# Optimization experiments

Measured on AMD Instinct MI355X. Metric: run time of the kernel, lower is better.

Reference implementation:

```python
import jax, jax.numpy as jnp
import numpy as np

B, N, IN_DIM, OUT_DIM, E = 2, 100000, 128, 128, 600000


def setup_inputs() -> dict:
    key = jax.random.key(0)
    ks = jax.random.split(key, 16)
    inp = {
        'x': jax.random.normal(ks[0], (B, N, IN_DIM), dtype=jnp.float32),
        'edges_r0': jax.random.randint(ks[1], (2, E), 0, N, dtype=jnp.int64),
        'edges_r1': jax.random.randint(ks[2], (2, E), 0, N, dtype=jnp.int64),
        'edges_r2': jax.random.randint(ks[3], (2, E), 0, N, dtype=jnp.int64),
    }
    s = 1.0 / np.sqrt(IN_DIM)
    for i in range(3):
        inp[f'w{i}'] = jax.random.uniform(ks[4 + 3 * i], (OUT_DIM, IN_DIM), minval=-s, maxval=s, dtype=jnp.float32)
        inp[f'gw{i}'] = jax.random.uniform(ks[5 + 3 * i], (2 * OUT_DIM, IN_DIM), minval=-s, maxval=s, dtype=jnp.float32)
        inp[f'gb{i}'] = jax.random.uniform(ks[6 + 3 * i], (2 * OUT_DIM,), minval=-s, maxval=s, dtype=jnp.float32)
    return inp


def _film_conv(x, edges_list, w_list, gw_list, gb_list):
    # x: (B,N,F). For each relation: gather src/dst, linear, FiLM, scatter_add on dst.
    Bn, Nn, _ = x.shape
    out = jnp.zeros((Bn, Nn, OUT_DIM), dtype=x.dtype)
    for edge_index, w, gw, gb in zip(edges_list, w_list, gw_list, gb_list):
        src, dst = edge_index[0], edge_index[1]
        x_src = x[:, src, :]                       # (B,E,F)
        msg_lin = jnp.einsum('bef,of->beo', x_src, w)
        x_dst = x[:, dst, :]                       # (B,E,F)
        film = jnp.einsum('bef,of->beo', x_dst, gw) + gb
        omega, mu = film[..., :OUT_DIM], film[..., OUT_DIM:]
        msg = jax.nn.relu(jax.nn.sigmoid(omega) * msg_lin + mu)
        out = out.at[:, dst, :].add(msg)
    return out


def reference(x, edges_r0, edges_r1, edges_r2, w0, w1, w2, gw0, gb0, gw1, gb1, gw2, gb2):
    return _film_conv(x, [edges_r0, edges_r1, edges_r2], [w0, w1, w2],
                      [gw0, gw1, gw2], [gb0, gb1, gb2])
```

## Files before the change

### kernel.cpp

```cpp
#include <hip/hip_runtime.h>

#define Bn 2
#define Nn 100000
#define DIM 128
#define En 600000
#define MTOT (Bn * Nn)
#define DPB 32

typedef __attribute__((ext_vector_type(8))) short bf16x8;
typedef __attribute__((ext_vector_type(4))) float f32x4;

__device__ __forceinline__ unsigned short f2bf(float f) {
    union { float f; unsigned u; } v; v.f = f;
    unsigned r = v.u + 0x7fffu + ((v.u >> 16) & 1u);
    return (unsigned short)(r >> 16);
}
__device__ __forceinline__ float bf2f(unsigned u16) {
    union { unsigned u; float f; } v; v.u = u16 << 16; return v.f;
}
__device__ __forceinline__ float bf_lo(unsigned u) {
    union { unsigned u; float f; } v; v.u = u << 16; return v.f;
}
__device__ __forceinline__ float bf_hi(unsigned u) {
    union { unsigned u; float f; } v; v.u = u & 0xffff0000u; return v.f;
}

__global__ __launch_bounds__(256) void cvt_x_kernel(const float4* __restrict__ x,
                                                    ushort4* __restrict__ xbf) {
    int i = blockIdx.x * 256 + threadIdx.x;
    float4 v = x[i];
    ushort4 o;
    o.x = f2bf(v.x); o.y = f2bf(v.y); o.z = f2bf(v.z); o.w = f2bf(v.w);
    xbf[i] = o;
}

__global__ __launch_bounds__(256) void cvt_w_kernel(
    const float* __restrict__ w0,  const float* __restrict__ gw0,
    const float* __restrict__ w1,  const float* __restrict__ gw1,
    const float* __restrict__ w2,  const float* __restrict__ gw2,
    unsigned short* __restrict__ WB)
{
    int idx = blockIdx.x * 256 + threadIdx.x;
    int r = idx / 49152;
    int j = idx - r * 49152;
    const float* w  = (r == 0) ? w0  : (r == 1 ? w1  : w2);
    const float* gw = (r == 0) ? gw0 : (r == 1 ? gw1 : gw2);
    float v = (j < 128 * 128) ? w[j] : gw[j - 128 * 128];
    WB[idx] = f2bf(v);
}

__global__ __launch_bounds__(256) void count_kernel(
    const int* __restrict__ e0, const int* __restrict__ e1, const int* __restrict__ e2,
    int* __restrict__ counts)
{
    int idx = blockIdx.x * 256 + threadIdx.x;
    if (idx >= 3 * En) return;
    int r = (idx >= 2 * En) ? 2 : (idx >= En ? 1 : 0);
    int e = idx - r * En;
    const int* ed = (r == 0) ? e0 : (r == 1 ? e1 : e2);
    int dst = ed[En + e];
    atomicAdd(&counts[r * Nn + dst], 1);
}

#define WPR 1563
__global__ __launch_bounds__(256) void alloc_kernel(
    const int* __restrict__ counts,
    int* __restrict__ starts,
    int* __restrict__ gcursor)
{
    int wid  = blockIdx.x * 4 + (threadIdx.x >> 6);
    int lane = threadIdx.x & 63;
    int r = wid / WPR;
    if (r >= 3) return;
    int dst = (wid - r * WPR) * 64 + lane;
    int c = (dst < Nn) ? counts[r * Nn + dst] : 0;

    int inc = c;
#pragma unroll
    for (int d = 1; d < 64; d <<= 1) {
        int v = __shfl_up(inc, d);
        if (lane >= d) inc += v;
    }
    int total = __shfl(inc, 63);
    int base = 0;
    if (lane == 63) base = atomicAdd(&gcursor[r], total);
    base = __shfl(base, 63);

    if (dst < Nn) starts[r * Nn + dst] = base + inc - c;
}

__global__ __launch_bounds__(256) void fill_kernel(
    const int* __restrict__ e0, const int* __restrict__ e1, const int* __restrict__ e2,
    const int* __restrict__ starts,
    int* __restrict__ cursor,
    int* __restrict__ records)
{
    int idx = blockIdx.x * 256 + threadIdx.x;
    if (idx >= 3 * En) return;
    int r = (idx >= 2 * En) ? 2 : (idx >= En ? 1 : 0);
    int e = idx - r * En;
    const int* ed = (r == 0) ? e0 : (r == 1 ? e1 : e2);
    int src = ed[e];
    int dst = ed[En + e];
    int pos = atomicAdd(&cursor[r * Nn + dst], 1);
    records[(size_t)r * En + starts[r * Nn + dst] + pos] = src;
}

__global__ __launch_bounds__(256) void transformA_kernel(
    const short* __restrict__ Xbf,
    const short* __restrict__ WB,
    unsigned short* __restrict__ Abuf)
{
    __shared__ unsigned short tile[64 * 128];
    const int tid  = threadIdx.x;
    const int wave = tid >> 6;
    const int lane = tid & 63;
    const int m = lane & 15;
    const int q = lane >> 4;
    const size_t nbase = (size_t)blockIdx.x * 64;

    bf16x8 a[4][4];
#pragma unroll
    for (int sub = 0; sub < 4; ++sub)
#pragma unroll
        for (int c = 0; c < 4; ++c)
            a[sub][c] = *(const bf16x8*)(Xbf + (nbase + (size_t)(sub * 16 + m)) * DIM + c * 32 + q * 8);

#pragma unroll
    for (int t = 0; t < 2; ++t) {
        const int ob = wave * 32 + t * 16;
        bf16x8 bfr[4];
#pragma unroll
        for (int c = 0; c < 4; ++c)
            bfr[c] = *(const bf16x8*)(WB + (size_t)(ob + m) * DIM + c * 32 + q * 8);

        const int o0 = ob + q * 4;
#pragma unroll
        for (int sub = 0; sub < 4; ++sub) {
            f32x4 acc = (f32x4){0.f, 0.f, 0.f, 0.f};
#pragma unroll
            for (int c = 0; c < 4; ++c)
                acc = __builtin_amdgcn_mfma_f32_16x16x32_bf16(bfr[c], a[sub][c], acc, 0, 0, 0);
            const int row = sub * 16 + m;
            ushort4 o4;
            o4.x = f2bf(acc[0]); o4.y = f2bf(acc[1]);
            o4.z = f2bf(acc[2]); o4.w = f2bf(acc[3]);
            *(ushort4*)&tile[row * 128 + (o0 ^ ((row & 7) << 3))] = o4;
        }
    }

    __syncthreads();

    const int r16 = tid >> 4;
    const int c8  = (tid & 15) * 8;
#pragma unroll
    for (int it = 0; it < 4; ++it) {
        const int row = it * 16 + r16;
        const int swz = (row & 7) << 3;
        const size_t node = nbase + (size_t)row;
        uint4 va = *(const uint4*)&tile[row * 128 + (c8 ^ swz)];
        *(uint4*)(Abuf + node * DIM + c8) = va;
    }
}

template <int FIRST>
__global__ __launch_bounds__(256) void film_accum_kernel(
    const short* __restrict__ Xbf,
    const short* __restrict__ GWB,
    const float* __restrict__ gb,
    const unsigned short* __restrict__ Abuf,
    const int* __restrict__ starts,
    const int* __restrict__ counts,
    const int* __restrict__ records,
    float* __restrict__ out)
{
    __shared__ unsigned short smtile[64 * 256];
    const int tid  = threadIdx.x;
    const int wave = tid >> 6;
    const int lane = tid & 63;
    const int m = lane & 15;
    const int q = lane >> 4;
    const int dbase = blockIdx.x * DPB;

    {
        bf16x8 a[4][4];
#pragma unroll
        for (int rt = 0; rt < 4; ++rt) {
            const int i = rt * 16 + m;
            const int b = i >> 5;
            const int local = i & 31;
            const size_t grow = (size_t)b * Nn + (size_t)(dbase + local);
#pragma unroll
            for (int c = 0; c < 4; ++c)
                a[rt][c] = *(const bf16x8*)(Xbf + grow * DIM + c * 32 + q * 8);
        }

        const int obase = wave * 64;
#pragma unroll
        for (int t = 0; t < 4; ++t) {
            const int ot = obase + t * 16;
            bf16x8 bfr[4];
#pragma unroll
            for (int c = 0; c < 4; ++c)
                bfr[c] = *(const bf16x8*)(GWB + (size_t)(ot + m) * DIM + c * 32 + q * 8);

            const int o0 = ot + q * 4;
            const float4 g = *(const float4*)(gb + o0);
#pragma unroll
            for (int rt = 0; rt < 4; ++rt) {
                f32x4 acc = (f32x4){0.f, 0.f, 0.f, 0.f};
#pragma unroll
                for (int c = 0; c < 4; ++c)
                    acc = __builtin_amdgcn_mfma_f32_16x16x32_bf16(bfr[c], a[rt][c], acc, 0, 0, 0);
                float v0 = acc[0] + g.x, v1 = acc[1] + g.y;
                float v2 = acc[2] + g.z, v3 = acc[3] + g.w;
                if (obase < 128) {
                    v0 = 1.f / (1.f + __expf(-v0));
                    v1 = 1.f / (1.f + __expf(-v1));
                    v2 = 1.f / (1.f + __expf(-v2));
                    v3 = 1.f / (1.f + __expf(-v3));
                }
                const int xrow = rt * 16 + m;
                ushort4 o4;
                o4.x = f2bf(v0); o4.y = f2bf(v1); o4.z = f2bf(v2); o4.w = f2bf(v3);
                *(ushort4*)&smtile[xrow * 256 + (o0 ^ ((xrow & 7) << 3))] = o4;
            }
        }
    }

    __syncthreads();

    const int half = lane >> 5;
    const int hl   = lane & 31;
    const int k    = hl * 4;
    const char* Abase = (const char*)(Abuf + (size_t)half * Nn * DIM + k);

    for (int ii = 0; ii < 8; ++ii) {
        const int dl  = wave * 8 + ii;
        const int dst = dbase + dl;
        const int cnt = counts[dst];
        if (!FIRST && cnt == 0) continue;
        const int beg = starts[dst];

        const int xrow = half * 32 + dl;
        const int swz  = (xrow & 7) << 3;
        const ushort4 sv = *(const ushort4*)&smtile[xrow * 256 + (k ^ swz)];
        const ushort4 mv = *(const ushort4*)&smtile[xrow * 256 + ((128 + k) ^ swz)];
        const float s0 = bf2f(sv.x), s1 = bf2f(sv.y), s2 = bf2f(sv.z), s3 = bf2f(sv.w);
        const float u0 = bf2f(mv.x), u1 = bf2f(mv.y), u2 = bf2f(mv.z), u3 = bf2f(mv.w);

        float a0 = 0.f, a1 = 0.f, a2 = 0.f, a3 = 0.f;
        float b0 = 0.f, b1 = 0.f, b2 = 0.f, b3 = 0.f;

        for (int base = 0; base < cnt; base += 64) {
            const int rem = cnt - base;
            const int nb  = rem < 64 ? rem : 64;
            int srcl = 0;
            if (lane < nb) srcl = records[beg + base + lane];

            int j = 0;
            for (; j + 1 < nb; j += 2) {
                const int sA = __builtin_amdgcn_readlane(srcl, j);
                const int sB = __builtin_amdgcn_readlane(srcl, j + 1);
                const uint2 avA = *(const uint2*)(Abase + (size_t)sA * (DIM * 2));
                const uint2 avB = *(const uint2*)(Abase + (size_t)sB * (DIM * 2));
                float r;
                r = fmaf(s0, bf_lo(avA.x), u0); a0 += fmaxf(r, 0.f);
                r = fmaf(s1, bf_hi(avA.x), u1); a1 += fmaxf(r, 0.f);
                r = fmaf(s2, bf_lo(avA.y), u2); a2 += fmaxf(r, 0.f);
                r = fmaf(s3, bf_hi(avA.y), u3); a3 += fmaxf(r, 0.f);
                r = fmaf(s0, bf_lo(avB.x), u0); b0 += fmaxf(r, 0.f);
                r = fmaf(s1, bf_hi(avB.x), u1); b1 += fmaxf(r, 0.f);
                r = fmaf(s2, bf_lo(avB.y), u2); b2 += fmaxf(r, 0.f);
                r = fmaf(s3, bf_hi(avB.y), u3); b3 += fmaxf(r, 0.f);
            }
            if (j < nb) {
                const int sA = __builtin_amdgcn_readlane(srcl, j);
                const uint2 avA = *(const uint2*)(Abase + (size_t)sA * (DIM * 2));
                float r;
                r = fmaf(s0, bf_lo(avA.x), u0); a0 += fmaxf(r, 0.f);
                r = fmaf(s1, bf_hi(avA.x), u1); a1 += fmaxf(r, 0.f);
                r = fmaf(s2, bf_lo(avA.y), u2); a2 += fmaxf(r, 0.f);
                r = fmaf(s3, bf_hi(avA.y), u3); a3 += fmaxf(r, 0.f);
            }
        }
        a0 += b0; a1 += b1; a2 += b2; a3 += b3;

        const size_t drow = ((size_t)half * Nn + (size_t)dst) * DIM;
        float4* op = (float4*)(out + drow + k);
        if (FIRST) {
            *op = make_float4(a0, a1, a2, a3);
        } else {
            float4 v = *op;
            v.x += a0; v.y += a1; v.z += a2; v.w += a3;
            *op = v;
        }
    }
}

__global__ __launch_bounds__(128) void fallback_kernel(
    const float* __restrict__ x,
    const int* __restrict__ edges,
    const float* __restrict__ w,
    const float* __restrict__ gw,
    const float* __restrict__ gb,
    float* __restrict__ out)
{
    __shared__ float xs[DIM], xd[DIM];
    int be = blockIdx.x;
    int e = be >> 1, b = be & 1;
    int t = threadIdx.x;
    int src = edges[e], dst = edges[En + e];
    xs[t] = x[((size_t)b * Nn + src) * DIM + t];
    xd[t] = x[((size_t)b * Nn + dst) * DIM + t];
    __syncthreads();
    float ml = 0.f, om = gb[t], mu = gb[128 + t];
    for (int kk = 0; kk < DIM; ++kk) {
        float xsk = xs[kk], xdk = xd[kk];
        ml += w[t * DIM + kk] * xsk;
        om += gw[t * DIM + kk] * xdk;
        mu += gw[(128 + t) * DIM + kk] * xdk;
    }
    float s = 1.f / (1.f + __expf(-om));
    float msg = s * ml + mu;
    msg = msg > 0.f ? msg : 0.f;
    unsafeAtomicAdd(out + ((size_t)b * Nn + dst) * DIM + t, msg);
}

extern "C" void kernel_launch(void* const* d_in, const int* in_sizes, int n_in,
                              void* d_out, int out_size, void* d_ws, size_t ws_size,
                              hipStream_t stream) {
    const float* x    = (const float*)d_in[0];
    const int*   ed[3] = { (const int*)d_in[1],
                           (const int*)d_in[2],
                           (const int*)d_in[3] };
    const float* w[3]  = { (const float*)d_in[4], (const float*)d_in[7], (const float*)d_in[10] };
    const float* gw[3] = { (const float*)d_in[5], (const float*)d_in[8], (const float*)d_in[11] };
    const float* gb[3] = { (const float*)d_in[6], (const float*)d_in[9], (const float*)d_in[12] };
    float* out = (float*)d_out;

    const size_t xbf_sz  = (size_t)MTOT * DIM * 2;
    const size_t wb_sz   = (size_t)3 * 384 * DIM * 2;
    const size_t buf_sz  = (size_t)MTOT * DIM * 2;
    const size_t cnt_sz  = (size_t)3 * Nn * 4;
    const size_t cur_sz  = (size_t)3 * Nn * 4;
    const size_t gcu_sz  = 64;
    const size_t sta_sz  = (size_t)3 * Nn * 4;
    const size_t rec_sz  = (size_t)3 * En * 4;
    const size_t need    = xbf_sz + wb_sz + buf_sz + cnt_sz + cur_sz + gcu_sz + sta_sz + rec_sz + 1024;

    if (ws_size >= need) {
        char* p = (char*)d_ws;
        short*          Xbf = (short*)p;              p += xbf_sz;
        unsigned short* WB  = (unsigned short*)p;     p += wb_sz;
        unsigned short* Ab  = (unsigned short*)p;     p += buf_sz;
        int*            counts  = (int*)p;            p += cnt_sz;
        int*            cursor  = (int*)p;            p += cur_sz;
        int*            gcursor = (int*)p;            p += gcu_sz;
        int*            starts  = (int*)p;            p += sta_sz;
        int*            records = (int*)p;

        hipMemsetAsync(counts, 0, cnt_sz + cur_sz + gcu_sz, stream);

        cvt_x_kernel<<<(MTOT * DIM / 4) / 256, 256, 0, stream>>>((const float4*)x, (ushort4*)Xbf);
        cvt_w_kernel<<<(3 * 384 * DIM) / 256, 256, 0, stream>>>(
            w[0], gw[0], w[1], gw[1], w[2], gw[2], WB);

        count_kernel<<<(3 * En + 255) / 256, 256, 0, stream>>>(ed[0], ed[1], ed[2], counts);
        alloc_kernel<<<(3 * WPR + 3) / 4, 256, 0, stream>>>(counts, starts, gcursor);
        fill_kernel<<<(3 * En + 255) / 256, 256, 0, stream>>>(ed[0], ed[1], ed[2], starts, cursor, records);

        for (int r = 0; r < 3; ++r) {
            const unsigned short* WBr  = WB + (size_t)r * 384 * DIM;
            const unsigned short* GWBr = WBr + (size_t)128 * DIM;
            transformA_kernel<<<MTOT / 64, 256, 0, stream>>>(
                Xbf, (const short*)WBr, Ab);
            const int* sta = starts + (size_t)r * Nn;
            const int* cnt = counts + (size_t)r * Nn;
            const int* rec = records + (size_t)r * En;
            if (r == 0)
                film_accum_kernel<1><<<Nn / DPB, 256, 0, stream>>>(
                    Xbf, (const short*)GWBr, gb[r], Ab, sta, cnt, rec, out);
            else
                film_accum_kernel<0><<<Nn / DPB, 256, 0, stream>>>(
                    Xbf, (const short*)GWBr, gb[r], Ab, sta, cnt, rec, out);
        }
    } else {
        hipMemsetAsync(d_out, 0, (size_t)MTOT * DIM * sizeof(float), stream);
        for (int r = 0; r < 3; ++r)
            fallback_kernel<<<En * Bn, 128, 0, stream>>>(x, ed[r], w[r], gw[r], gb[r], out);
    }
}
```

Measured before the change: 920.8 us.

## Fuse three per-relation transforms into one kernel and halve destinations per block

The three per-relation transformA launches are merged into one kernel that reads each X tile once and computes all three W projections into a triple-sized A buffer. Separately, the film_accum kernel now handles 16 destinations per block instead of 32, which shrinks shared memory and register use and doubles the grid. The aim is to cut repeated X reads and launch overhead and to improve occupancy and load balance in the gather phase. In exchange it needs three times the intermediate workspace, a larger LDS tile in the transform kernel, and more blocks that each redo the FiLM GEMM setup.

Result: faster. 862.3 us (-6.4%).

```diff
diff --git a/kernel.cpp b/kernel.cpp
--- a/kernel.cpp
+++ b/kernel.cpp
@@ -5,7 +5,7 @@
 #define DIM 128
 #define En 600000
 #define MTOT (Bn * Nn)
-#define DPB 32
+#define DPB 16
 
 typedef __attribute__((ext_vector_type(8))) short bf16x8;
 typedef __attribute__((ext_vector_type(4))) float f32x4;
@@ -106,12 +106,12 @@
     records[(size_t)r * En + starts[r * Nn + dst] + pos] = src;
 }
 
-__global__ __launch_bounds__(256) void transformA_kernel(
+__global__ __launch_bounds__(256) void transformA_all_kernel(
     const short* __restrict__ Xbf,
     const short* __restrict__ WB,
     unsigned short* __restrict__ Abuf)
 {
-    __shared__ unsigned short tile[64 * 128];
+    __shared__ unsigned short tile[64 * 384];
     const int tid  = threadIdx.x;
     const int wave = tid >> 6;
     const int lane = tid & 63;
@@ -127,14 +127,16 @@
             a[sub][c] = *(const bf16x8*)(Xbf + (nbase + (size_t)(sub * 16 + m)) * DIM + c * 32 + q * 8);
 
 #pragma unroll
-    for (int t = 0; t < 2; ++t) {
-        const int ob = wave * 32 + t * 16;
+    for (int t = 0; t < 6; ++t) {
+        const int widx = wave * 96 + t * 16;
+        const int r    = widx >> 7;
+        const int o    = widx & 127;
         bf16x8 bfr[4];
 #pragma unroll
         for (int c = 0; c < 4; ++c)
-            bfr[c] = *(const bf16x8*)(WB + (size_t)(ob + m) * DIM + c * 32 + q * 8);
-
-        const int o0 = ob + q * 4;
+            bfr[c] = *(const bf16x8*)(WB + (size_t)(r * 384 + o + m) * DIM + c * 32 + q * 8);
+
+        const int o0 = widx + q * 4;
 #pragma unroll
         for (int sub = 0; sub < 4; ++sub) {
             f32x4 acc = (f32x4){0.f, 0.f, 0.f, 0.f};
@@ -145,7 +147,7 @@
             ushort4 o4;
             o4.x = f2bf(acc[0]); o4.y = f2bf(acc[1]);
             o4.z = f2bf(acc[2]); o4.w = f2bf(acc[3]);
-            *(ushort4*)&tile[row * 128 + (o0 ^ ((row & 7) << 3))] = o4;
+            *(ushort4*)&tile[row * 384 + (o0 ^ ((row & 7) << 3))] = o4;
         }
     }
 
@@ -158,8 +160,11 @@
         const int row = it * 16 + r16;
         const int swz = (row & 7) << 3;
         const size_t node = nbase + (size_t)row;
-        uint4 va = *(const uint4*)&tile[row * 128 + (c8 ^ swz)];
-        *(uint4*)(Abuf + node * DIM + c8) = va;
+#pragma unroll
+        for (int r = 0; r < 3; ++r) {
+            uint4 va = *(const uint4*)&tile[row * 384 + ((r * 128 + c8) ^ swz)];
+            *(uint4*)(Abuf + (size_t)r * MTOT * DIM + node * DIM + c8) = va;
+        }
     }
 }
 
@@ -174,7 +179,7 @@
     const int* __restrict__ records,
     float* __restrict__ out)
 {
-    __shared__ unsigned short smtile[64 * 256];
+    __shared__ unsigned short smtile[32 * 256];
     const int tid  = threadIdx.x;
     const int wave = tid >> 6;
     const int lane = tid & 63;
@@ -183,12 +188,12 @@
     const int dbase = blockIdx.x * DPB;
 
     {
-        bf16x8 a[4][4];
-#pragma unroll
-        for (int rt = 0; rt < 4; ++rt) {
+        bf16x8 a[2][4];
+#pragma unroll
+        for (int rt = 0; rt < 2; ++rt) {
             const int i = rt * 16 + m;
-            const int b = i >> 5;
-            const int local = i & 31;
+            const int b = i >> 4;
+            const int local = i & 15;
             const size_t grow = (size_t)b * Nn + (size_t)(dbase + local);
 #pragma unroll
             for (int c = 0; c < 4; ++c)
@@ -207,7 +212,7 @@
             const int o0 = ot + q * 4;
             const float4 g = *(const float4*)(gb + o0);
 #pragma unroll
-            for (int rt = 0; rt < 4; ++rt) {
+            for (int rt = 0; rt < 2; ++rt) {
                 f32x4 acc = (f32x4){0.f, 0.f, 0.f, 0.f};
 #pragma unroll
                 for (int c = 0; c < 4; ++c)
@@ -235,14 +240,14 @@
     const int k    = hl * 4;
     const char* Abase = (const char*)(Abuf + (size_t)half * Nn * DIM + k);
 
-    for (int ii = 0; ii < 8; ++ii) {
-        const int dl  = wave * 8 + ii;
+    for (int ii = 0; ii < 4; ++ii) {
+        const int dl  = wave * 4 + ii;
         const int dst = dbase + dl;
         const int cnt = counts[dst];
         if (!FIRST && cnt == 0) continue;
         const int beg = starts[dst];
 
-        const int xrow = half * 32 + dl;
+        const int xrow = half * 16 + dl;
         const int swz  = (xrow & 7) << 3;
         const ushort4 sv = *(const ushort4*)&smtile[xrow * 256 + (k ^ swz)];
         const ushort4 mv = *(const ushort4*)&smtile[xrow * 256 + ((128 + k) ^ swz)];
@@ -347,13 +352,13 @@
     const size_t gcu_sz  = 64;
     const size_t sta_sz  = (size_t)3 * Nn * 4;
     const size_t rec_sz  = (size_t)3 * En * 4;
-    const size_t need    = xbf_sz + wb_sz + buf_sz + cnt_sz + cur_sz + gcu_sz + sta_sz + rec_sz + 1024;
+    const size_t need    = xbf_sz + wb_sz + 3 * buf_sz + cnt_sz + cur_sz + gcu_sz + sta_sz + rec_sz + 1024;
 
     if (ws_size >= need) {
         char* p = (char*)d_ws;
         short*          Xbf = (short*)p;              p += xbf_sz;
         unsigned short* WB  = (unsigned short*)p;     p += wb_sz;
-        unsigned short* Ab  = (unsigned short*)p;     p += buf_sz;
+        unsigned short* Ab  = (unsigned short*)p;     p += 3 * buf_sz;
         int*            counts  = (int*)p;            p += cnt_sz;
         int*            cursor  = (int*)p;            p += cur_sz;
         int*            gcursor = (int*)p;            p += gcu_sz;
@@ -370,20 +375,21 @@
         alloc_kernel<<<(3 * WPR + 3) / 4, 256, 0, stream>>>(counts, starts, gcursor);
         fill_kernel<<<(3 * En + 255) / 256, 256, 0, stream>>>(ed[0], ed[1], ed[2], starts, cursor, records);
 
+        transformA_all_kernel<<<MTOT / 64, 256, 0, stream>>>(
+            Xbf, (const short*)WB, Ab);
+
         for (int r = 0; r < 3; ++r) {
-            const unsigned short* WBr  = WB + (size_t)r * 384 * DIM;
-            const unsigned short* GWBr = WBr + (size_t)128 * DIM;
-            transformA_kernel<<<MTOT / 64, 256, 0, stream>>>(
-                Xbf, (const short*)WBr, Ab);
+            const unsigned short* GWBr = WB + (size_t)r * 384 * DIM + (size_t)128 * DIM;
+            const unsigned short* Abr  = Ab + (size_t)r * MTOT * DIM;
             const int* sta = starts + (size_t)r * Nn;
             const int* cnt = counts + (size_t)r * Nn;
             const int* rec = records + (size_t)r * En;
             if (r == 0)
                 film_accum_kernel<1><<<Nn / DPB, 256, 0, stream>>>(
-                    Xbf, (const short*)GWBr, gb[r], Ab, sta, cnt, rec, out);
+                    Xbf, (const short*)GWBr, gb[r], Abr, sta, cnt, rec, out);
             else
                 film_accum_kernel<0><<<Nn / DPB, 256, 0, stream>>>(
-                    Xbf, (const short*)GWBr, gb[r], Ab, sta, cnt, rec, out);
+                    Xbf, (const short*)GWBr, gb[r], Abr, sta, cnt, rec, out);
         }
     } else {
         hipMemsetAsync(d_out, 0, (size_t)MTOT * DIM * sizeof(float), stream);
```
